# Performance work log

Measured on AMD Instinct MI355X. Metric: run time of the kernel, lower is better.

The kernel has to match this reference:

```python
import jax, jax.numpy as jnp
import numpy as np

N_ATOMS = 500000
N_BONDS = 1000000
MAX_NB = 6
ATOM_FDIM = 133
BOND_FDIM = 14
HIDDEN = 128
MP_DEPTH = 3
ATOMS_PER_MOL = 20


def setup_inputs() -> dict:
    key = jax.random.key(0)
    ks = jax.random.split(key, 12)
    inp = {
        "f_atoms": jax.random.normal(ks[0], (N_ATOMS, ATOM_FDIM), jnp.float32),
        "f_bonds": jax.random.normal(ks[1], (N_BONDS, BOND_FDIM), jnp.float32),
        "Wi_w": jax.random.normal(ks[2], (HIDDEN, ATOM_FDIM), jnp.float32) * 0.05,
        "Wi_b": jax.random.normal(ks[3], (HIDDEN,), jnp.float32) * 0.05,
        "Wh_w": jax.random.normal(ks[4], (HIDDEN, HIDDEN + BOND_FDIM), jnp.float32) * 0.05,
        "Wh_b": jax.random.normal(ks[5], (HIDDEN,), jnp.float32) * 0.05,
        "Wo_w": jax.random.normal(ks[6], (HIDDEN, ATOM_FDIM + HIDDEN), jnp.float32) * 0.05,
        "Wo_b": jax.random.normal(ks[7], (HIDDEN,), jnp.float32) * 0.05,
        "ffn_w": jax.random.normal(ks[8], (1, HIDDEN), jnp.float32) * 0.05,
        "ffn_b": jax.random.normal(ks[9], (1,), jnp.float32) * 0.05,
        "a2a": jax.random.randint(ks[10], (N_ATOMS, MAX_NB), 0, N_ATOMS, jnp.int32),
        "a2b": jax.random.randint(ks[11], (N_ATOMS, MAX_NB), 0, N_BONDS, jnp.int32),
        "atoms_per_mol": ATOMS_PER_MOL,
    }
    return inp


def reference(f_atoms, f_bonds, Wi_w, Wi_b, Wh_w, Wh_b, Wo_w, Wo_b, ffn_w, ffn_b,
              a2a, a2b, atoms_per_mol):
    # W_i + ReLU: initial atom messages
    x = f_atoms @ Wi_w.T + Wi_b                     # [N_atoms, H]
    message = jax.nn.relu(x)
    # pre-aggregate bond features once (constant across depths)
    nei_f_bonds_sum = f_bonds[a2b].sum(axis=1)      # [N_atoms, BOND_FDIM]
    for _ in range(MP_DEPTH - 1):
        # gather neighbor messages and sum (index_select_ND + sum(dim=1));
        # concat(msg_gather, bond_gather).sum(1) == concat(sum(msg), sum(bond))
        nei_a_message = message[a2a].sum(axis=1)    # [N_atoms, H]
        nei = jnp.concatenate([nei_a_message, nei_f_bonds_sum], axis=1)
        message = jax.nn.relu(x + nei @ Wh_w.T + Wh_b)
        # dropout is identity in eval mode
    # final aggregation + W_o
    a_message = message[a2a].sum(axis=1)            # [N_atoms, H]
    a_input = jnp.concatenate([f_atoms, a_message], axis=1)
    atom_hiddens = jax.nn.relu(a_input @ Wo_w.T + Wo_b)
    # max readout per molecule (equal-size a_scope of atoms_per_mol)
    n_atoms, h = atom_hiddens.shape
    mol_vecs = atom_hiddens.reshape(n_atoms // atoms_per_mol, atoms_per_mol, h).max(axis=1)
    # FFN head (NN_depth=1): Dropout (identity) + Linear(H -> 1)
    return mol_vecs @ ffn_w.T + ffn_b               # [n_mols, 1]
```

## Files before the change

kernel.cpp:

```cpp
#include <hip/hip_runtime.h>
#include <hip/hip_bf16.h>

#define N_ATOMS   500000
#define N_BONDS   1000000
#define MAX_NB    6
#define ATOM_FDIM 133
#define BOND_FDIM 14
#define HIDDEN    128
#define N_MOLS    25000
#define APM       20

typedef __attribute__((ext_vector_type(8))) short short8;
typedef __attribute__((ext_vector_type(4))) float f32x4;
typedef unsigned short u16;
typedef unsigned int   u32;

__device__ __forceinline__ float bf2f(u16 u) {
    u32 t = ((u32)u) << 16;
    return __builtin_bit_cast(float, t);
}
__device__ __forceinline__ u16 f2bf(float f) {
    u32 t = __builtin_bit_cast(u32, f);
    t += 0x7FFFu + ((t >> 16) & 1u);
    return (u16)(t >> 16);
}
__device__ __forceinline__ u32 pk2(float a, float b) {
    return (u32)f2bf(a) | ((u32)f2bf(b) << 16);
}

__device__ __forceinline__ void gl16(const u16* g, u16* l) {
    __builtin_amdgcn_global_load_lds(
        (__attribute__((address_space(1))) void*)(g),
        (__attribute__((address_space(3))) void*)(l), 16, 0, 0);
}

__global__ void prep_weights(const float* __restrict__ Wi, const float* __restrict__ Wh,
                             const float* __restrict__ Wo,
                             u16* __restrict__ Wip, u16* __restrict__ Whp, u16* __restrict__ Wop) {
    int stride = gridDim.x * blockDim.x;
    int tid = blockIdx.x * blockDim.x + threadIdx.x;
    for (int i = tid; i < 128 * 160; i += stride) {
        int r = i / 160, c = i % 160;
        Wip[i] = (c < 133) ? f2bf(Wi[r * 133 + c]) : (u16)0;
        Whp[i] = (c < 142) ? f2bf(Wh[r * 142 + c]) : (u16)0;
    }
    for (int i = tid; i < 128 * 288; i += stride) {
        int r = i / 288, c = i % 288;
        float v = 0.f;
        if (c < 133)      v = Wo[r * 261 + c];
        else if (c >= 160) v = Wo[r * 261 + (c - 27)];
        Wop[i] = f2bf(v);
    }
}

__global__ __launch_bounds__(256) void bond_gather(const float* __restrict__ fb, const int* __restrict__ a2b,
                                                   u16* __restrict__ outp) {
    long t = (long)blockIdx.x * 256 + threadIdx.x;
    int atom = (int)(t >> 4);
    int c2   = (int)(t & 15);
    if (atom >= N_ATOMS) return;
    int c0 = 2 * c2, c1 = c0 + 1;
    float s0 = 0.f, s1 = 0.f;
    if (c0 < BOND_FDIM) {
#pragma unroll
        for (int j = 0; j < MAX_NB; j++) {
            int idx = a2b[atom * 6 + j];
            const float* row = fb + (long)idx * BOND_FDIM;
            s0 += row[c0];
            if (c1 < BOND_FDIM) s1 += row[c1];
        }
    }
    *(u32*)(outp + (long)atom * 32 + c0) = pk2(s0, s1);
}

__global__ __launch_bounds__(256) void gather_relu_sum(const u16* __restrict__ src,
                                                       const int* __restrict__ a2a,
                                                       u16* __restrict__ dst) {
    long t = (long)blockIdx.x * 256 + threadIdx.x;
    int atom = (int)(t >> 4);
    int c8   = (int)(t & 15) << 3;
    float s[8] = {0, 0, 0, 0, 0, 0, 0, 0};
#pragma unroll
    for (int j = 0; j < MAX_NB; j++) {
        int idx = a2a[atom * 6 + j];
        uint4 v = *(const uint4*)(src + (long)idx * 128 + c8);
        u32 w[4] = {v.x, v.y, v.z, v.w};
#pragma unroll
        for (int q = 0; q < 4; q++) {
            s[2 * q]     += fmaxf(__builtin_bit_cast(float, w[q] << 16), 0.f);
            s[2 * q + 1] += fmaxf(__builtin_bit_cast(float, w[q] & 0xFFFF0000u), 0.f);
        }
    }
    uint4 o;
    o.x = pk2(s[0], s[1]);
    o.y = pk2(s[2], s[3]);
    o.z = pk2(s[4], s[5]);
    o.w = pk2(s[6], s[7]);
    *(uint4*)(dst + (long)atom * 128 + c8) = o;
}

#define ISSUE_SLOT(d, t)                                                              \
    do {                                                                              \
        long r_ = (t) * TILE + wave * 16 + lrow;                                      \
        if (r_ > N_ATOMS - 1) r_ = N_ATOMS - 1;                                       \
        u16* ab_ = AL + ((d) * WAVES + wave) * (KB0 * 512);                           \
        {                                                                             \
            const u16* p_ = A0 + r_ * (long)ldA0 + kg * 8;                            \
            _Pragma("unroll") for (int kb = 0; kb < KB0; kb++)                        \
                gl16(p_ + kb * 32, ab_ + kb * 512);                                   \
        }                                                                             \
        if constexpr (KB1 > 0) {                                                      \
            const u16* p_ = A1 + r_ * (long)ldA1 + kg * 8;                            \
            _Pragma("unroll") for (int kb = 0; kb < KB1; kb++)                        \
                a1v[d][kb] = *(const uint4*)(p_ + kb * 32);                           \
        }                                                                             \
        if constexpr (ADDX) {                                                         \
            _Pragma("unroll") for (int n = 0; n < 8; n++)                             \
                xv[d][n] = *(const uint2*)(Xadd + r_ * 128 + n * 16 + kg * 4);        \
        }                                                                             \
    } while (0)

template <int KB0, int KB1, bool ADDX, bool BIAS, int WAVES>
__global__ __launch_bounds__(WAVES * 64) void gemm_dma(
    const u16* __restrict__ A0, int ldA0,
    const u16* __restrict__ A1, int ldA1,
    const u16* __restrict__ Wp, const float* __restrict__ bias,
    const u16* __restrict__ Xadd, u16* __restrict__ Out) {
    constexpr int KB    = KB0 + KB1;
    constexpr int KP    = KB * 32;
    constexpr int TILE  = WAVES * 16;
    constexpr long NT   = (N_ATOMS + TILE - 1) / TILE;
    constexpr int WSLOTS = KB * 8;
    constexpr int DEPTH = 2;
    constexpr int NWAIT = KB0 + (KB1 > 0 ? KB1 : 0) + (ADDX ? 8 : 0) + 4;
    static_assert(NWAIT <= 63, "vmcnt range");
    __shared__ __align__(16) u16 lds[WSLOTS * 512 + DEPTH * WAVES * KB0 * 512 + WAVES * 2048];

    const int lane = threadIdx.x & 63;
    const int wave = threadIdx.x >> 6;
    const int lrow = lane & 15;
    const int kg   = lane >> 4;

    u16* WL = lds;
    u16* AL = lds + WSLOTS * 512;
    u16* SB = lds + WSLOTS * 512 + DEPTH * WAVES * KB0 * 512;

    for (int s = wave; s < WSLOTS; s += WAVES) {
        int kb = s >> 3, n = s & 7;
        gl16(Wp + (n * 16 + lrow) * KP + kb * 32 + kg * 8, WL + s * 512);
    }
    asm volatile("s_waitcnt vmcnt(0)" ::: "memory");
    __syncthreads();

    float4 b4[8];
#pragma unroll
    for (int n = 0; n < 8; n++)
        b4[n] = BIAS ? *(const float4*)(bias + n * 16 + kg * 4) : (float4){0.f, 0.f, 0.f, 0.f};

    const int G  = gridDim.x;
    const long t0 = blockIdx.x;

    uint4 a1v[DEPTH][KB1 > 0 ? KB1 : 1];
    uint2 xv[DEPTH][ADDX ? 8 : 1];

#pragma unroll
    for (int d = 0; d < DEPTH; d++) ISSUE_SLOT(d, t0 + (long)d * G);
    __builtin_amdgcn_sched_barrier(0);

#pragma unroll 1
    for (long tt = t0; tt < NT; tt += (long)DEPTH * G) {
#pragma unroll
        for (int d = 0; d < DEPTH; d++) {
            long t = tt + (long)d * G;
            if (t < NT) {
                asm volatile("s_waitcnt vmcnt(%0)" :: "n"(NWAIT) : "memory");
                __builtin_amdgcn_sched_barrier(0);

                const u16* ab = AL + (d * WAVES + wave) * (KB0 * 512);
                f32x4 acc[8];
#pragma unroll
                for (int n = 0; n < 8; n++) acc[n] = (f32x4){0.f, 0.f, 0.f, 0.f};
#pragma unroll
                for (int kb = 0; kb < KB; kb++) {
                    short8 af;
                    if (kb < KB0) af = *(const short8*)(ab + kb * 512 + lane * 8);
                    else          af = __builtin_bit_cast(short8, a1v[d][(kb - KB0) < KB1 ? (kb - KB0) : 0]);
#pragma unroll
                    for (int n = 0; n < 8; n++) {
                        short8 bf = *(const short8*)(WL + (kb * 8 + n) * 512 + lane * 8);
                        acc[n] = __builtin_amdgcn_mfma_f32_16x16x32_bf16(bf, af, acc[n], 0, 0, 0);
                    }
                }

                const long wrow0 = t * TILE + wave * 16;
                if (wrow0 < N_ATOMS) {
                    u16* sb = SB + wave * 2048;
#pragma unroll
                    for (int n = 0; n < 8; n++) {
                        float v0 = acc[n][0] + b4[n].x;
                        float v1 = acc[n][1] + b4[n].y;
                        float v2 = acc[n][2] + b4[n].z;
                        float v3 = acc[n][3] + b4[n].w;
                        if constexpr (ADDX) {
                            v0 += __builtin_bit_cast(float, xv[d][n].x << 16);
                            v1 += __builtin_bit_cast(float, xv[d][n].x & 0xFFFF0000u);
                            v2 += __builtin_bit_cast(float, xv[d][n].y << 16);
                            v3 += __builtin_bit_cast(float, xv[d][n].y & 0xFFFF0000u);
                        }
                        uint2 o;
                        o.x = pk2(v0, v1);
                        o.y = pk2(v2, v3);
                        int sboff = lrow * 256 + ((n * 32 + kg * 8) ^ ((lrow & 7) << 4));
                        *(uint2*)(sb + (sboff >> 1)) = o;
                    }
#pragma unroll
                    for (int i = 0; i < 4; i++) {
                        int R = i * 4 + (lane >> 4);
                        int B = ((lane & 15) * 16) ^ ((R & 7) << 4);
                        uint4 v = *(const uint4*)(sb + ((R * 256 + B) >> 1));
                        *(uint4*)(Out + wrow0 * 128 + i * 512 + lane * 8) = v;
                    }
                }
                __builtin_amdgcn_sched_barrier(0);
                ISSUE_SLOT(d, t + (long)DEPTH * G);
                __builtin_amdgcn_sched_barrier(0);
            }
        }
    }
}

__global__ __launch_bounds__(512, 2) void gemm_wi(
    const float* __restrict__ FA, const u16* __restrict__ Wp,
    const float* __restrict__ bias, u16* __restrict__ fa16, u16* __restrict__ Out) {
    constexpr int KB = 5, KP = 160, TILE = 128;
    constexpr long NT = (N_ATOMS + TILE - 1) / TILE;
    constexpr int WSLOTS = KB * 8;
    constexpr int DEPTH = 2;
    constexpr int NWAIT = 23;
    __shared__ __align__(16) u16 WL[WSLOTS * 512];

    const int lane = threadIdx.x & 63;
    const int wave = threadIdx.x >> 6;
    const int lrow = lane & 15;
    const int kg   = lane >> 4;

    for (int s = wave; s < WSLOTS; s += 8) {
        int kb = s >> 3, n = s & 7;
        gl16(Wp + (n * 16 + lrow) * KP + kb * 32 + kg * 8, WL + s * 512);
    }
    asm volatile("s_waitcnt vmcnt(0)" ::: "memory");
    __syncthreads();

    float4 b4[8];
#pragma unroll
    for (int n = 0; n < 8; n++) b4[n] = *(const float4*)(bias + n * 16 + kg * 4);

    const int G  = gridDim.x;
    const long t0 = blockIdx.x;

    uint4 af32[DEPTH][4][2];
    uint4 a4[DEPTH];
    float a4s[DEPTH];

#define WI_ISSUE(d, t)                                                         \
    do {                                                                       \
        long r_ = (t) * TILE + wave * 16 + lrow;                               \
        if (r_ > N_ATOMS - 1) r_ = N_ATOMS - 1;                                \
        const float* p_ = FA + r_ * (long)ATOM_FDIM + kg * 8;                  \
        _Pragma("unroll") for (int kb = 0; kb < 4; kb++) {                     \
            af32[d][kb][0] = *(const uint4*)(p_ + kb * 32);                    \
            af32[d][kb][1] = *(const uint4*)(p_ + kb * 32 + 4);                \
        }                                                                      \
        if (kg == 0) {                                                         \
            const float* q_ = FA + r_ * (long)ATOM_FDIM + 128;                 \
            a4[d]  = *(const uint4*)(q_);                                      \
            a4s[d] = q_[4];                                                    \
        }                                                                      \
    } while (0)

#pragma unroll
    for (int d = 0; d < DEPTH; d++) WI_ISSUE(d, t0 + (long)d * G);
    __builtin_amdgcn_sched_barrier(0);

#pragma unroll 1
    for (long tt = t0; tt < NT; tt += (long)DEPTH * G) {
#pragma unroll
        for (int d = 0; d < DEPTH; d++) {
            long t = tt + (long)d * G;
            if (t < NT) {
                asm volatile("s_waitcnt vmcnt(%0)" :: "n"(NWAIT) : "memory");
                __builtin_amdgcn_sched_barrier(0);

                long r = t * TILE + wave * 16 + lrow;
                bool wr = (r < N_ATOMS);

                short8 frag[5];
#pragma unroll
                for (int kb = 0; kb < 4; kb++) {
                    float4 lo = __builtin_bit_cast(float4, af32[d][kb][0]);
                    float4 hi = __builtin_bit_cast(float4, af32[d][kb][1]);
                    uint4 pk;
                    pk.x = pk2(lo.x, lo.y);
                    pk.y = pk2(lo.z, lo.w);
                    pk.z = pk2(hi.x, hi.y);
                    pk.w = pk2(hi.z, hi.w);
                    frag[kb] = __builtin_bit_cast(short8, pk);
                }
                {
                    uint4 pk = (uint4){0, 0, 0, 0};
                    if (kg == 0) {
                        float4 q = __builtin_bit_cast(float4, a4[d]);
                        pk.x = pk2(q.x, q.y);
                        pk.y = pk2(q.z, q.w);
                        pk.z = pk2(a4s[d], 0.f);
                    }
                    frag[4] = __builtin_bit_cast(short8, pk);
                }

                f32x4 acc[8];
#pragma unroll
                for (int n = 0; n < 8; n++) acc[n] = (f32x4){0.f, 0.f, 0.f, 0.f};
#pragma unroll
                for (int kb = 0; kb < 5; kb++) {
#pragma unroll
                    for (int n = 0; n < 8; n++) {
                        short8 bf = *(const short8*)(WL + (kb * 8 + n) * 512 + lane * 8);
                        acc[n] = __builtin_amdgcn_mfma_f32_16x16x32_bf16(bf, frag[kb], acc[n], 0, 0, 0);
                    }
                }

                if (wr) {
#pragma unroll
                    for (int kb = 0; kb < 5; kb++)
                        *(uint4*)(fa16 + r * 160 + kb * 32 + kg * 8) = __builtin_bit_cast(uint4, frag[kb]);
#pragma unroll
                    for (int n = 0; n < 8; n++) {
                        uint2 o;
                        o.x = pk2(acc[n][0] + b4[n].x, acc[n][1] + b4[n].y);
                        o.y = pk2(acc[n][2] + b4[n].z, acc[n][3] + b4[n].w);
                        *(uint2*)(Out + r * 128 + n * 16 + kg * 4) = o;
                    }
                }
                __builtin_amdgcn_sched_barrier(0);
                WI_ISSUE(d, t + (long)DEPTH * G);
                __builtin_amdgcn_sched_barrier(0);
            }
        }
    }
#undef WI_ISSUE
}

__global__ __launch_bounds__(256) void readout(const u16* __restrict__ ah,
                                               const float* __restrict__ ffn_w,
                                               const float* __restrict__ ffn_b,
                                               float* __restrict__ out) {
    int mol  = blockIdx.x * 4 + (threadIdx.x >> 6);
    int lane = threadIdx.x & 63;
    if (mol >= N_MOLS) return;
    float m0 = -1e30f, m1 = -1e30f;
    const u16* base = ah + (long)mol * APM * 128 + 2 * lane;
#pragma unroll
    for (int a = 0; a < APM; a++) {
        u32 v = *(const u32*)(base + a * 128);
        m0 = fmaxf(m0, bf2f((u16)(v & 0xFFFFu)));
        m1 = fmaxf(m1, bf2f((u16)(v >> 16)));
    }
    m0 = fmaxf(m0, 0.f);
    m1 = fmaxf(m1, 0.f);
    float p = m0 * ffn_w[2 * lane] + m1 * ffn_w[2 * lane + 1];
#pragma unroll
    for (int off = 32; off > 0; off >>= 1) p += __shfl_down(p, off);
    if (lane == 0) out[mol] = p + ffn_b[0];
}

extern "C" void kernel_launch(void* const* d_in, const int* in_sizes, int n_in,
                              void* d_out, int out_size, void* d_ws, size_t ws_size,
                              hipStream_t stream) {
    const float* f_atoms = (const float*)d_in[0];
    const float* f_bonds = (const float*)d_in[1];
    const float* Wi_w = (const float*)d_in[2];
    const float* Wi_b = (const float*)d_in[3];
    const float* Wh_w = (const float*)d_in[4];
    const float* Wh_b = (const float*)d_in[5];
    const float* Wo_w = (const float*)d_in[6];
    const float* Wo_b = (const float*)d_in[7];
    const float* ffn_w = (const float*)d_in[8];
    const float* ffn_b = (const float*)d_in[9];
    const int* a2a = (const int*)d_in[10];
    const int* a2b = (const int*)d_in[11];
    float* out = (float*)d_out;

    char* ws = (char*)d_ws;
    u16* fa    = (u16*)(ws);
    u16* xb    = (u16*)(ws + 160000000L);
    u16* msgA  = (u16*)(ws + 288000000L);
    u16* msgB  = (u16*)(ws + 416000000L);
    u16* nsum  = (u16*)(ws + 544000000L);
    u16* nbond = (u16*)(ws + 672000000L);
    u16* Wip   = (u16*)(ws + 704000000L);
    u16* Whp   = (u16*)(ws + 704040960L);
    u16* Wop   = (u16*)(ws + 704081920L);

    prep_weights<<<64, 256, 0, stream>>>(Wi_w, Wh_w, Wo_w, Wip, Whp, Wop);
    bond_gather<<<31250, 256, 0, stream>>>(f_bonds, a2b, nbond);

    gemm_wi<<<256, 512, 0, stream>>>(f_atoms, Wip, Wi_b, fa, xb);

    gather_relu_sum<<<31250, 256, 0, stream>>>(xb, a2a, nsum);
    gemm_dma<4, 1, true, true, 8><<<256, 512, 0, stream>>>(
        nsum, 128, nbond, 32, Whp, Wh_b, xb, msgA);
    gather_relu_sum<<<31250, 256, 0, stream>>>(msgA, a2a, nsum);
    gemm_dma<4, 1, true, true, 8><<<256, 512, 0, stream>>>(
        nsum, 128, nbond, 32, Whp, Wh_b, xb, msgB);
    gather_relu_sum<<<31250, 256, 0, stream>>>(msgB, a2a, nsum);
    gemm_dma<5, 4, false, true, 6><<<256, 384, 0, stream>>>(
        fa, 160, nsum, 128, Wop, Wo_b, (const u16*)nullptr, msgA);

    readout<<<6250, 256, 0, stream>>>(msgA, ffn_w, ffn_b, out);
}
```

Before: 813.9 us.

## Fuse W_o GEMM with per-molecule max readout and FFN head

Replaces the final W_o GEMM and the separate readout kernel with one kernel. Each wave handles one molecule (20 atoms as two 16-row MFMA tiles), applies bias+ReLU, does the max over atoms via shuffles, and dots with the FFN weights, writing one scalar per molecule. This removes the write and re-read of the 500k x 128 atom_hiddens buffer and one launch. The cost is that the second tile of 16 rows is mostly padding (only 4 of its rows are real), so some MFMA work is wasted, and the new pipeline uses fewer threads per block than the old GEMM.

Result: slower. 834.1 us (+2.5%).

```diff
diff --git a/kernel.cpp b/kernel.cpp
--- a/kernel.cpp
+++ b/kernel.cpp
@@ -229,6 +229,129 @@
     }
 }
 
+__global__ __launch_bounds__(256) void gemm_wo_fused(
+    const u16* __restrict__ fa, const u16* __restrict__ nsum,
+    const u16* __restrict__ Wp, const float* __restrict__ bias,
+    const float* __restrict__ ffn_w, const float* __restrict__ ffn_b,
+    float* __restrict__ out) {
+    constexpr int KB0 = 5, KB1 = 4, KB = 9, KP = 288;
+    constexpr int WAVES = 4, DEPTH = 2;
+    constexpr int WSLOTS = KB * 8;
+    constexpr int NWAIT = 2 * KB0 + 2 * KB1 + 1;
+    __shared__ __align__(16) u16 lds[WSLOTS * 512 + DEPTH * WAVES * 2 * KB0 * 512];
+
+    const int lane = threadIdx.x & 63;
+    const int wave = threadIdx.x >> 6;
+    const int lrow = lane & 15;
+    const int kg   = lane >> 4;
+
+    u16* WL = lds;
+    u16* AL = lds + WSLOTS * 512;
+
+    for (int s = wave; s < WSLOTS; s += WAVES) {
+        int kb = s >> 3, n = s & 7;
+        gl16(Wp + (n * 16 + lrow) * KP + kb * 32 + kg * 8, WL + s * 512);
+    }
+    asm volatile("s_waitcnt vmcnt(0)" ::: "memory");
+    __syncthreads();
+
+    f32x4 bb[8], fw[8];
+#pragma unroll
+    for (int n = 0; n < 8; n++) {
+        bb[n] = __builtin_bit_cast(f32x4, *(const float4*)(bias + n * 16 + kg * 4));
+        fw[n] = __builtin_bit_cast(f32x4, *(const float4*)(ffn_w + n * 16 + kg * 4));
+    }
+    const float fb0 = ffn_b[0];
+
+    const long TOTW = (long)gridDim.x * WAVES;
+    const long w0   = (long)blockIdx.x * WAVES + wave;
+
+    uint4 a1v[DEPTH][2][KB1];
+
+    auto issue = [&](int d, long m) {
+        long mm = (m < N_MOLS) ? m : (N_MOLS - 1);
+        long base = mm * APM;
+        long r0 = base + lrow;
+        long r1 = base + 16 + (lrow & 3);
+        u16* ab = AL + ((d * WAVES + wave) * (2 * KB0)) * 512;
+        const u16* p0 = fa + r0 * 160 + kg * 8;
+#pragma unroll
+        for (int kb = 0; kb < KB0; kb++) gl16(p0 + kb * 32, ab + kb * 512);
+        const u16* p1 = fa + r1 * 160 + kg * 8;
+#pragma unroll
+        for (int kb = 0; kb < KB0; kb++) gl16(p1 + kb * 32, ab + (KB0 + kb) * 512);
+        const u16* q0 = nsum + r0 * 128 + kg * 8;
+#pragma unroll
+        for (int kb = 0; kb < KB1; kb++) a1v[d][0][kb] = *(const uint4*)(q0 + kb * 32);
+        const u16* q1 = nsum + r1 * 128 + kg * 8;
+#pragma unroll
+        for (int kb = 0; kb < KB1; kb++) a1v[d][1][kb] = *(const uint4*)(q1 + kb * 32);
+    };
+
+#pragma unroll
+    for (int d = 0; d < DEPTH; d++) issue(d, w0 + (long)d * TOTW);
+    __builtin_amdgcn_sched_barrier(0);
+
+#pragma unroll 1
+    for (long mm0 = w0; mm0 < N_MOLS; mm0 += (long)DEPTH * TOTW) {
+#pragma unroll
+        for (int d = 0; d < DEPTH; d++) {
+            long m = mm0 + (long)d * TOTW;
+            if (m < N_MOLS) {
+                asm volatile("s_waitcnt vmcnt(%0)" :: "n"(NWAIT) : "memory");
+                __builtin_amdgcn_sched_barrier(0);
+
+                const u16* ab = AL + ((d * WAVES + wave) * (2 * KB0)) * 512;
+                f32x4 acc0[8], acc1[8];
+#pragma unroll
+                for (int n = 0; n < 8; n++) {
+                    acc0[n] = (f32x4){0.f, 0.f, 0.f, 0.f};
+                    acc1[n] = (f32x4){0.f, 0.f, 0.f, 0.f};
+                }
+#pragma unroll
+                for (int kb = 0; kb < KB; kb++) {
+                    short8 af0, af1;
+                    if (kb < KB0) {
+                        af0 = *(const short8*)(ab + kb * 512 + lane * 8);
+                        af1 = *(const short8*)(ab + (KB0 + kb) * 512 + lane * 8);
+                    } else {
+                        af0 = __builtin_bit_cast(short8, a1v[d][0][(kb - KB0) < KB1 ? (kb - KB0) : 0]);
+                        af1 = __builtin_bit_cast(short8, a1v[d][1][(kb - KB0) < KB1 ? (kb - KB0) : 0]);
+                    }
+#pragma unroll
+                    for (int n = 0; n < 8; n++) {
+                        short8 bf = *(const short8*)(WL + (kb * 8 + n) * 512 + lane * 8);
+                        acc0[n] = __builtin_amdgcn_mfma_f32_16x16x32_bf16(bf, af0, acc0[n], 0, 0, 0);
+                        acc1[n] = __builtin_amdgcn_mfma_f32_16x16x32_bf16(bf, af1, acc1[n], 0, 0, 0);
+                    }
+                }
+
+                float part = 0.f;
+#pragma unroll
+                for (int n = 0; n < 8; n++) {
+#pragma unroll
+                    for (int j = 0; j < 4; j++) {
+                        float w = fmaxf(acc0[n][j] + bb[n][j], 0.f);
+                        w = fmaxf(w, fmaxf(acc1[n][j] + bb[n][j], 0.f));
+#pragma unroll
+                        for (int sft = 1; sft <= 8; sft <<= 1)
+                            w = fmaxf(w, __shfl_xor(w, sft, 64));
+                        part += w * fw[n][j];
+                    }
+                }
+                part += __shfl_xor(part, 16, 64);
+                part += __shfl_xor(part, 32, 64);
+                if (lane == 0) out[m] = part + fb0;
+
+                __builtin_amdgcn_sched_barrier(0);
+                issue(d, m + (long)DEPTH * TOTW);
+                __builtin_amdgcn_sched_barrier(0);
+            }
+        }
+    }
+    asm volatile("s_waitcnt vmcnt(0)" ::: "memory");
+}
+
 __global__ __launch_bounds__(512, 2) void gemm_wi(
     const float* __restrict__ FA, const u16* __restrict__ Wp,
     const float* __restrict__ bias, u16* __restrict__ fa16, u16* __restrict__ Out) {
@@ -348,29 +471,6 @@
         }
     }
 #undef WI_ISSUE
-}
-
-__global__ __launch_bounds__(256) void readout(const u16* __restrict__ ah,
-                                               const float* __restrict__ ffn_w,
-                                               const float* __restrict__ ffn_b,
-                                               float* __restrict__ out) {
-    int mol  = blockIdx.x * 4 + (threadIdx.x >> 6);
-    int lane = threadIdx.x & 63;
-    if (mol >= N_MOLS) return;
-    float m0 = -1e30f, m1 = -1e30f;
-    const u16* base = ah + (long)mol * APM * 128 + 2 * lane;
-#pragma unroll
-    for (int a = 0; a < APM; a++) {
-        u32 v = *(const u32*)(base + a * 128);
-        m0 = fmaxf(m0, bf2f((u16)(v & 0xFFFFu)));
-        m1 = fmaxf(m1, bf2f((u16)(v >> 16)));
-    }
-    m0 = fmaxf(m0, 0.f);
-    m1 = fmaxf(m1, 0.f);
-    float p = m0 * ffn_w[2 * lane] + m1 * ffn_w[2 * lane + 1];
-#pragma unroll
-    for (int off = 32; off > 0; off >>= 1) p += __shfl_down(p, off);
-    if (lane == 0) out[mol] = p + ffn_b[0];
 }
 
 extern "C" void kernel_launch(void* const* d_in, const int* in_sizes, int n_in,
@@ -413,8 +513,5 @@
     gemm_dma<4, 1, true, true, 8><<<256, 512, 0, stream>>>(
         nsum, 128, nbond, 32, Whp, Wh_b, xb, msgB);
     gather_relu_sum<<<31250, 256, 0, stream>>>(msgB, a2a, nsum);
-    gemm_dma<5, 4, false, true, 6><<<256, 384, 0, stream>>>(
-        fa, 160, nsum, 128, Wop, Wo_b, (const u16*)nullptr, msgA);
-
-    readout<<<6250, 256, 0, stream>>>(msgA, ffn_w, ffn_b, out);
-}
+    gemm_wo_fused<<<256, 256, 0, stream>>>(fa, nsum, Wop, Wo_b, ffn_w, ffn_b, out);
+}
```

## Fuse Wo GEMM with per-molecule max readout and FFN head

Applied to the files above, without the earlier changes.

Replaces the final Wo GEMM plus separate readout kernel with one kernel. It computes 80-row tiles (4 molecules), applies bias and ReLU, stages results in LDS, then does the max-pool and dot with ffn_w in-block. This removes the write and reread of the 500k x 128 atom-hidden tensor and one launch. In exchange it uses a different tile and pipeline design (5 waves, 250 blocks) with extra barriers per tile, which could lower GEMM efficiency.

New measurement: 820.2 us. About the same (+0.8%).

```diff
diff --git a/kernel.cpp b/kernel.cpp
--- a/kernel.cpp
+++ b/kernel.cpp
@@ -229,6 +229,129 @@
     }
 }
 
+__global__ __launch_bounds__(320) void gemm_wo_red(
+    const u16* __restrict__ fa, const u16* __restrict__ nsum,
+    const u16* __restrict__ Wp, const float* __restrict__ bias,
+    const float* __restrict__ ffn_w, const float* __restrict__ ffn_b,
+    float* __restrict__ out) {
+    constexpr int KB0 = 5, KB1 = 4, KB = 9, KP = 288;
+    constexpr int WAVES = 5, DEPTH = 2, TILE = 80;
+    constexpr long NT = N_MOLS / 4;
+    constexpr int WSLOTS = KB * 8;
+    constexpr int NWAIT = KB0 + KB1 + 1;
+    __shared__ __align__(16) u16 lds[WSLOTS * 512 + DEPTH * WAVES * KB0 * 512 + 80 * 128];
+
+    const int lane = threadIdx.x & 63;
+    const int wave = threadIdx.x >> 6;
+    const int lrow = lane & 15;
+    const int kg   = lane >> 4;
+
+    u16* WL  = lds;
+    u16* AL  = lds + WSLOTS * 512;
+    u16* RED = lds + WSLOTS * 512 + DEPTH * WAVES * KB0 * 512;
+
+    for (int s = wave; s < WSLOTS; s += WAVES) {
+        int kb = s >> 3, n = s & 7;
+        gl16(Wp + (n * 16 + lrow) * KP + kb * 32 + kg * 8, WL + s * 512);
+    }
+    asm volatile("s_waitcnt vmcnt(0)" ::: "memory");
+    __syncthreads();
+
+    f32x4 bb[8];
+#pragma unroll
+    for (int n = 0; n < 8; n++)
+        bb[n] = __builtin_bit_cast(f32x4, *(const float4*)(bias + n * 16 + kg * 4));
+    float fw0 = ffn_w[2 * lane], fw1 = ffn_w[2 * lane + 1];
+    const float fb0 = ffn_b[0];
+
+    const int G  = gridDim.x;
+    const long t0 = blockIdx.x;
+
+    uint4 a1v[DEPTH][KB1];
+
+    auto issue = [&](int d, long t) {
+        long tc = (t < NT) ? t : (NT - 1);
+        long r = tc * TILE + wave * 16 + lrow;
+        u16* ab = AL + ((d * WAVES + wave) * KB0) * 512;
+        const u16* p = fa + r * 160 + kg * 8;
+#pragma unroll
+        for (int kb = 0; kb < KB0; kb++) gl16(p + kb * 32, ab + kb * 512);
+        const u16* q = nsum + r * 128 + kg * 8;
+#pragma unroll
+        for (int kb = 0; kb < KB1; kb++) a1v[d][kb] = *(const uint4*)(q + kb * 32);
+    };
+
+#pragma unroll
+    for (int d = 0; d < DEPTH; d++) issue(d, t0 + (long)d * G);
+    __builtin_amdgcn_sched_barrier(0);
+
+#pragma unroll 1
+    for (long tt = t0; tt < NT; tt += (long)DEPTH * G) {
+#pragma unroll
+        for (int d = 0; d < DEPTH; d++) {
+            long t = tt + (long)d * G;
+            if (t < NT) {
+                asm volatile("s_waitcnt vmcnt(%0)" :: "n"(NWAIT) : "memory");
+                __builtin_amdgcn_sched_barrier(0);
+
+                const u16* ab = AL + ((d * WAVES + wave) * KB0) * 512;
+                f32x4 acc[8];
+#pragma unroll
+                for (int n = 0; n < 8; n++) acc[n] = (f32x4){0.f, 0.f, 0.f, 0.f};
+#pragma unroll
+                for (int kb = 0; kb < KB; kb++) {
+                    short8 af;
+                    if (kb < KB0) af = *(const short8*)(ab + kb * 512 + lane * 8);
+                    else          af = __builtin_bit_cast(short8, a1v[d][(kb - KB0) < KB1 ? (kb - KB0) : 0]);
+#pragma unroll
+                    for (int n = 0; n < 8; n++) {
+                        short8 bf = *(const short8*)(WL + (kb * 8 + n) * 512 + lane * 8);
+                        acc[n] = __builtin_amdgcn_mfma_f32_16x16x32_bf16(bf, af, acc[n], 0, 0, 0);
+                    }
+                }
+
+                const int lr = wave * 16 + lrow;
+#pragma unroll
+                for (int n = 0; n < 8; n++) {
+                    float v0 = fmaxf(acc[n][0] + bb[n][0], 0.f);
+                    float v1 = fmaxf(acc[n][1] + bb[n][1], 0.f);
+                    float v2 = fmaxf(acc[n][2] + bb[n][2], 0.f);
+                    float v3 = fmaxf(acc[n][3] + bb[n][3], 0.f);
+                    uint2 o;
+                    o.x = pk2(v0, v1);
+                    o.y = pk2(v2, v3);
+                    int boff = lr * 256 + ((n * 32 + kg * 8) ^ ((lr & 7) << 4));
+                    *(uint2*)(RED + (boff >> 1)) = o;
+                }
+                asm volatile("s_waitcnt lgkmcnt(0)" ::: "memory");
+                __builtin_amdgcn_sched_barrier(0);
+                __builtin_amdgcn_s_barrier();
+
+                if (wave < 4) {
+                    float m0 = 0.f, m1 = 0.f;
+#pragma unroll
+                    for (int a = 0; a < APM; a++) {
+                        int rr = wave * APM + a;
+                        int boff = rr * 256 + ((4 * lane) ^ ((rr & 7) << 4));
+                        u32 v = *(const u32*)(RED + (boff >> 1));
+                        m0 = fmaxf(m0, bf2f((u16)(v & 0xFFFFu)));
+                        m1 = fmaxf(m1, bf2f((u16)(v >> 16)));
+                    }
+                    float p = m0 * fw0 + m1 * fw1;
+#pragma unroll
+                    for (int sft = 1; sft <= 32; sft <<= 1) p += __shfl_xor(p, sft, 64);
+                    if (lane == 0) out[t * 4 + wave] = p + fb0;
+                }
+                __builtin_amdgcn_s_barrier();
+
+                __builtin_amdgcn_sched_barrier(0);
+                issue(d, t + (long)DEPTH * G);
+                __builtin_amdgcn_sched_barrier(0);
+            }
+        }
+    }
+}
+
 __global__ __launch_bounds__(512, 2) void gemm_wi(
     const float* __restrict__ FA, const u16* __restrict__ Wp,
     const float* __restrict__ bias, u16* __restrict__ fa16, u16* __restrict__ Out) {
@@ -348,29 +471,6 @@
         }
     }
 #undef WI_ISSUE
-}
-
-__global__ __launch_bounds__(256) void readout(const u16* __restrict__ ah,
-                                               const float* __restrict__ ffn_w,
-                                               const float* __restrict__ ffn_b,
-                                               float* __restrict__ out) {
-    int mol  = blockIdx.x * 4 + (threadIdx.x >> 6);
-    int lane = threadIdx.x & 63;
-    if (mol >= N_MOLS) return;
-    float m0 = -1e30f, m1 = -1e30f;
-    const u16* base = ah + (long)mol * APM * 128 + 2 * lane;
-#pragma unroll
-    for (int a = 0; a < APM; a++) {
-        u32 v = *(const u32*)(base + a * 128);
-        m0 = fmaxf(m0, bf2f((u16)(v & 0xFFFFu)));
-        m1 = fmaxf(m1, bf2f((u16)(v >> 16)));
-    }
-    m0 = fmaxf(m0, 0.f);
-    m1 = fmaxf(m1, 0.f);
-    float p = m0 * ffn_w[2 * lane] + m1 * ffn_w[2 * lane + 1];
-#pragma unroll
-    for (int off = 32; off > 0; off >>= 1) p += __shfl_down(p, off);
-    if (lane == 0) out[mol] = p + ffn_b[0];
 }
 
 extern "C" void kernel_launch(void* const* d_in, const int* in_sizes, int n_in,
@@ -413,8 +513,5 @@
     gemm_dma<4, 1, true, true, 8><<<256, 512, 0, stream>>>(
         nsum, 128, nbond, 32, Whp, Wh_b, xb, msgB);
     gather_relu_sum<<<31250, 256, 0, stream>>>(msgB, a2a, nsum);
-    gemm_dma<5, 4, false, true, 6><<<256, 384, 0, stream>>>(
-        fa, 160, nsum, 128, Wop, Wo_b, (const u16*)nullptr, msgA);
-
-    readout<<<6250, 256, 0, stream>>>(msgA, ffn_w, ffn_b, out);
-}
+    gemm_wo_red<<<250, 320, 0, stream>>>(fa, nsum, Wop, Wo_b, ffn_w, ffn_b, out);
+}
```

## Fuse first neighbor gather-relu-sum into the Wh GEMM kernel

Applied to the files above, without the earlier changes.

Adds a gemm_gwh kernel that gathers the six neighbor rows of the message pool, applies ReLU and sums them in registers, then feeds the result directly as MFMA fragments with bond sums and Wh weights held in LDS. The output adds bias and the residual x and is written through a swizzled LDS staging buffer. Only the first message-passing depth uses it. It removes one gather launch and the write and re-read of the intermediate neighbor-sum buffer, but the GEMM now stalls on random gathers with no software pipelining to hide that latency.

After: 814.5 us. No clear change (+0.1%).

```diff
diff --git a/kernel.cpp b/kernel.cpp
--- a/kernel.cpp
+++ b/kernel.cpp
@@ -12,6 +12,7 @@
 
 typedef __attribute__((ext_vector_type(8))) short short8;
 typedef __attribute__((ext_vector_type(4))) float f32x4;
+typedef __attribute__((ext_vector_type(4))) unsigned int u32x4;
 typedef unsigned short u16;
 typedef unsigned int   u32;
 
@@ -97,6 +98,116 @@
     o.z = pk2(s[4], s[5]);
     o.w = pk2(s[6], s[7]);
     *(uint4*)(dst + (long)atom * 128 + c8) = o;
+}
+
+__global__ __launch_bounds__(512, 4) void gemm_gwh(
+    const u16* __restrict__ pool, const int* __restrict__ a2a,
+    const u16* __restrict__ nbond, const u16* __restrict__ Wp,
+    const float* __restrict__ bias, u16* __restrict__ Out) {
+    constexpr int KB = 5, KP = 160;
+    constexpr int WAVES = 8, TILE = 128;
+    constexpr long NT = (N_ATOMS + TILE - 1) / TILE;
+    constexpr int WSLOTS = KB * 8;
+    __shared__ __align__(16) u16 lds[WSLOTS * 512 + WAVES * 2048];
+
+    const int lane = threadIdx.x & 63;
+    const int wave = threadIdx.x >> 6;
+    const int lrow = lane & 15;
+    const int kg   = lane >> 4;
+
+    u16* WL = lds;
+    u16* SB = lds + WSLOTS * 512;
+
+    for (int s = wave; s < WSLOTS; s += WAVES) {
+        int kb = s >> 3, n = s & 7;
+        gl16(Wp + (n * 16 + lrow) * KP + kb * 32 + kg * 8, WL + s * 512);
+    }
+    asm volatile("s_waitcnt vmcnt(0)" ::: "memory");
+    __syncthreads();
+
+    float4 b4[8];
+#pragma unroll
+    for (int n = 0; n < 8; n++) b4[n] = *(const float4*)(bias + n * 16 + kg * 4);
+
+    const int G = gridDim.x;
+#pragma unroll 1
+    for (long t = blockIdx.x; t < NT; t += G) {
+        long r = t * TILE + wave * 16 + lrow;
+        if (r > N_ATOMS - 1) r = N_ATOMS - 1;
+
+        const int* ip = a2a + r * 6;
+        uint2 i01 = *(const uint2*)(ip);
+        uint2 i23 = *(const uint2*)(ip + 2);
+        uint2 i45 = *(const uint2*)(ip + 4);
+        u32 idx[6] = {i01.x, i01.y, i23.x, i23.y, i45.x, i45.y};
+
+        short8 frag[5];
+#pragma unroll
+        for (int p = 0; p < 4; p++) {
+            uint4 g[6];
+#pragma unroll
+            for (int j = 0; j < 6; j++)
+                g[j] = *(const uint4*)(pool + (long)idx[j] * 128 + p * 32 + kg * 8);
+            float s[8] = {0, 0, 0, 0, 0, 0, 0, 0};
+#pragma unroll
+            for (int j = 0; j < 6; j++) {
+                u32 w4[4] = {g[j].x, g[j].y, g[j].z, g[j].w};
+#pragma unroll
+                for (int q = 0; q < 4; q++) {
+                    s[2 * q]     += fmaxf(__builtin_bit_cast(float, w4[q] << 16), 0.f);
+                    s[2 * q + 1] += fmaxf(__builtin_bit_cast(float, w4[q] & 0xFFFF0000u), 0.f);
+                }
+            }
+            uint4 pk;
+            pk.x = pk2(s[0], s[1]);
+            pk.y = pk2(s[2], s[3]);
+            pk.z = pk2(s[4], s[5]);
+            pk.w = pk2(s[6], s[7]);
+            frag[p] = __builtin_bit_cast(short8, pk);
+        }
+        frag[4] = __builtin_bit_cast(short8, *(const uint4*)(nbond + r * 32 + kg * 8));
+
+        uint2 xv[8];
+#pragma unroll
+        for (int n = 0; n < 8; n++)
+            xv[n] = *(const uint2*)(pool + r * 128 + n * 16 + kg * 4);
+
+        f32x4 acc[8];
+#pragma unroll
+        for (int n = 0; n < 8; n++) acc[n] = (f32x4){0.f, 0.f, 0.f, 0.f};
+#pragma unroll
+        for (int kb = 0; kb < 5; kb++) {
+#pragma unroll
+            for (int n = 0; n < 8; n++) {
+                short8 bf = *(const short8*)(WL + (kb * 8 + n) * 512 + lane * 8);
+                acc[n] = __builtin_amdgcn_mfma_f32_16x16x32_bf16(bf, frag[kb], acc[n], 0, 0, 0);
+            }
+        }
+
+        const long wrow0 = t * TILE + wave * 16;
+        if (wrow0 < N_ATOMS) {
+            u16* sb = SB + wave * 2048;
+#pragma unroll
+            for (int n = 0; n < 8; n++) {
+                float v0 = acc[n][0] + b4[n].x + __builtin_bit_cast(float, xv[n].x << 16);
+                float v1 = acc[n][1] + b4[n].y + __builtin_bit_cast(float, xv[n].x & 0xFFFF0000u);
+                float v2 = acc[n][2] + b4[n].z + __builtin_bit_cast(float, xv[n].y << 16);
+                float v3 = acc[n][3] + b4[n].w + __builtin_bit_cast(float, xv[n].y & 0xFFFF0000u);
+                uint2 o;
+                o.x = pk2(v0, v1);
+                o.y = pk2(v2, v3);
+                int sboff = lrow * 256 + ((n * 32 + kg * 8) ^ ((lrow & 7) << 4));
+                *(uint2*)(sb + (sboff >> 1)) = o;
+            }
+#pragma unroll
+            for (int i = 0; i < 4; i++) {
+                int R = i * 4 + (lane >> 4);
+                int B = ((lane & 15) * 16) ^ ((R & 7) << 4);
+                u32x4 v = *(const u32x4*)(sb + ((R * 256 + B) >> 1));
+                __builtin_nontemporal_store(v, (u32x4*)(Out + wrow0 * 128 + i * 512 + lane * 8));
+            }
+        }
+    }
 }
 
 #define ISSUE_SLOT(d, t)                                                              \
@@ -406,12 +517,12 @@
 
     gemm_wi<<<256, 512, 0, stream>>>(f_atoms, Wip, Wi_b, fa, xb);
 
-    gather_relu_sum<<<31250, 256, 0, stream>>>(xb, a2a, nsum);
-    gemm_dma<4, 1, true, true, 8><<<256, 512, 0, stream>>>(
-        nsum, 128, nbond, 32, Whp, Wh_b, xb, msgA);
+    gemm_gwh<<<512, 512, 0, stream>>>(xb, a2a, nbond, Whp, Wh_b, msgA);
+
     gather_relu_sum<<<31250, 256, 0, stream>>>(msgA, a2a, nsum);
     gemm_dma<4, 1, true, true, 8><<<256, 512, 0, stream>>>(
         nsum, 128, nbond, 32, Whp, Wh_b, xb, msgB);
+
     gather_relu_sum<<<31250, 256, 0, stream>>>(msgB, a2a, nsum);
     gemm_dma<5, 4, false, true, 6><<<256, 384, 0, stream>>>(
         fa, 160, nsum, 128, Wop, Wo_b, (const u16*)nullptr, msgA);
```
